# Kernel optimization log

Measured on AMD Instinct MI355X. Metric: run time of the kernel, lower is better.

The kernel has to match this reference:

```python
import jax, jax.numpy as jnp
import numpy as np
from functools import partial

TEMP = 0.07
BN_EPS = 1e-5


def conv1x1(W, x):
    # W: (c_out, c_in), x: (b, c_in, t, h, w) -> (b, c_out, t, h, w)
    return jnp.einsum('oc,bcthw->bothw', W, x)


def dwconv3d(x, W, spatial_dilation):
    # depthwise conv3d, kernel (9,3,3), temporal pad 4, spatial pad = dilation
    rc = x.shape[1]
    d = spatial_dilation
    return jax.lax.conv_general_dilated(
        x, W,
        window_strides=(1, 1, 1),
        padding=[(4, 4), (d, d), (d, d)],
        rhs_dilation=(1, d, d),
        feature_group_count=rc,
        dimension_numbers=('NCDHW', 'OIDHW', 'NCDHW'))


def sk_feat(nx, nseq, seq):
    # nx, nseq, seq: (b, c, t, n). Torch einsum 'bthh,bcth->bcth' takes the
    # DIAGONAL of softmax(aff/T, axis=-1); compute it via logsumexp without
    # materializing the softmax matrix.
    aff = jnp.einsum('bctn,bctm->btnm', nx, nseq) / TEMP          # (b,t,n,n)
    lse = jax.nn.logsumexp(aff, axis=-1)                           # (b,t,n)
    diag = jnp.einsum('bctn,bctn->btn', nx, nseq) / TEMP           # (b,t,n)
    diag_sm = jnp.exp(diag - lse)                                  # (b,t,n)
    return diag_sm[:, None, :, :] * seq                            # (b,c,t,n)


def shift_prev(x):  # seq1: [x[:, :, :1], x[:, :, :-1]]
    return jnp.concatenate([x[:, :, :1], x[:, :, :-1]], axis=2)


def shift_next(x):  # seq2: [x[:, :, 1:], x[:, :, -1:]]
    return jnp.concatenate([x[:, :, 1:], x[:, :, -1:]], axis=2)


def forward(x, W_dc2, W_up2, W_dc, W_sa1, W_sa2, W_sa3, W_back, gamma, beta):
    shortcut = x
    x = conv1x1(W_dc2, x)                                          # (b,c,t,h,w)
    norm = jnp.sqrt(jnp.sum(x * x, axis=1, keepdims=True))
    nx = x / jnp.maximum(norm, 1e-12)                              # F.normalize dim=1
    b, c, t, h, w = x.shape
    n = h * w
    x4 = x.reshape(b, c, t, n)
    nx4 = nx.reshape(b, c, t, n)

    third = jnp.float32(1.0 / 3.0)  # weights2 = ones(3)/3, non-trainable
    feats = (sk_feat(nx4, shift_prev(nx4), shift_prev(x4)) * third
             + sk_feat(nx4, shift_next(nx4), shift_next(x4)) * third
             + sk_feat(nx4, nx4, x4) * third)
    feats = feats.reshape(b, c, t, h, w)

    xx = conv1x1(W_dc, x)                                          # (b, rc, t, h, w)
    agg = (dwconv3d(xx, W_sa1, 1) * third
           + dwconv3d(xx, W_sa2, 2) * third
           + dwconv3d(xx, W_sa3, 3) * third)
    score = jax.nn.relu(conv1x1(W_back, agg))                      # (b,c,t,h,w)

    feats = conv1x1(W_up2, feats * score)
    y = shortcut + feats

    # BatchNorm3d (training-mode batch statistics, biased variance)
    mean = jnp.mean(y, axis=(0, 2, 3, 4), keepdims=True)
    var = jnp.mean((y - mean) ** 2, axis=(0, 2, 3, 4), keepdims=True)
    g = gamma[None, :, None, None, None]
    bta = beta[None, :, None, None, None]
    y = g * (y - mean) / jnp.sqrt(var + BN_EPS) + bta
    return jax.nn.relu(y)


def setup_inputs() -> dict:
    key = jax.random.key(0)
    ks = jax.random.split(key, 10)
    c = 256
    rc = c // 4
    b, t, h, w = 4, 8, 28, 28
    s = 0.05
    return {
        'x': jax.random.normal(ks[0], (b, c, t, h, w), dtype=jnp.float32),
        'W_dc2': jax.random.normal(ks[1], (c, c), dtype=jnp.float32) * s,
        'W_up2': jax.random.normal(ks[2], (c, c), dtype=jnp.float32) * s,
        'W_dc': jax.random.normal(ks[3], (rc, c), dtype=jnp.float32) * s,
        'W_sa1': jax.random.normal(ks[4], (rc, 1, 9, 3, 3), dtype=jnp.float32) * s,
        'W_sa2': jax.random.normal(ks[5], (rc, 1, 9, 3, 3), dtype=jnp.float32) * s,
        'W_sa3': jax.random.normal(ks[6], (rc, 1, 9, 3, 3), dtype=jnp.float32) * s,
        'W_back': jax.random.normal(ks[7], (c, rc), dtype=jnp.float32) * s,
        'gamma': jax.random.uniform(ks[8], (c,), dtype=jnp.float32, minval=0.5, maxval=1.5),
        'beta': jax.random.normal(ks[9], (c,), dtype=jnp.float32) * s,
    }


def reference(x, W_dc2, W_up2, W_dc, W_sa1, W_sa2, W_sa3, W_back, gamma, beta):
    return forward(x, W_dc2, W_up2, W_dc, W_sa1, W_sa2, W_sa3, W_back, gamma, beta)
```

## Files before the change

kernel.cpp:

```cpp
#include <hip/hip_runtime.h>

#define B_ 4
#define C_ 256
#define T_ 8
#define HW_ 784
#define RC_ 64
#define TNH (T_*HW_)
#define BT_ (B_*T_)
#define TEMP_INV 14.28571428571f

typedef __attribute__((ext_vector_type(8))) short bf16x8;
typedef __attribute__((ext_vector_type(4))) float f32x4;

__device__ __forceinline__ ushort f2bf(float f) {
    uint x = __float_as_uint(f);
    uint r = (x + 0x7FFFu + ((x >> 16) & 1u)) >> 16;
    return (ushort)r;
}

#define GL2LDS16(g, l) __builtin_amdgcn_global_load_lds( \
    (const __attribute__((address_space(1))) void*)(g), \
    (__attribute__((address_space(3))) void*)(l), 16, 0, 0)

__global__ __launch_bounds__(256) void k_wcvt(
    const float* __restrict__ w_dc2, const float* __restrict__ w_up2,
    const float* __restrict__ w_dc, const float* __restrict__ w_back,
    ushort* __restrict__ dst)
{
    const int idx = blockIdx.x * 256 + threadIdx.x;
    if (idx >= 163840) return;
    float v;
    if (idx < 65536)       v = w_dc2[idx];
    else if (idx < 131072) v = w_up2[idx - 65536];
    else if (idx < 147456) v = w_dc[idx - 131072];
    else                   v = w_back[idx - 147456];
    dst[idx] = f2bf(v);
}

__global__ __launch_bounds__(256) void k_xpose(
    const float* __restrict__ X, ushort* __restrict__ XT)
{
    __shared__ float xs[256][17];
    const int sl = blockIdx.y, b = sl >> 3, t = sl & 7;
    const int n0 = blockIdx.x * 16;
    const int tid = threadIdx.x;
    {
        const int n_l = tid & 15;
        const int c0 = tid >> 4;
        const float* p = X + (b * C_ * T_ + c0 * T_ + t) * HW_ + n0 + n_l;
        #pragma unroll
        for (int i = 0; i < 16; ++i)
            xs[c0 + 16 * i][n_l] = p[(size_t)16 * i * TNH];
    }
    __syncthreads();
    const int n_l = tid >> 4;
    const int cq = tid & 15;
    union { ushort u[16]; uint4 q[2]; } o;
    #pragma unroll
    for (int i = 0; i < 16; ++i)
        o.u[i] = f2bf(xs[cq * 16 + i][n_l]);
    uint4* dst = (uint4*)(XT + ((size_t)(sl * HW_ + n0 + n_l)) * 256 + cq * 16);
    dst[0] = o.q[0];
    dst[1] = o.q[1];
}

__global__ __launch_bounds__(256) void k_xpose64(
    const float* __restrict__ A, ushort* __restrict__ AT)
{
    __shared__ float xs[64][17];
    const int sl = blockIdx.y, b = sl >> 3, t = sl & 7;
    const int n0 = blockIdx.x * 16;
    const int tid = threadIdx.x;
    {
        const int n_l = tid & 15;
        const int c0 = tid >> 4;
        #pragma unroll
        for (int i = 0; i < 4; ++i)
            xs[c0 + 16 * i][n_l] = A[((size_t)(b * RC_ + c0 + 16 * i) * T_ + t) * HW_ + n0 + n_l];
    }
    __syncthreads();
    const int n_l = tid >> 4;
    const int cq = tid & 15;
    union { ushort u[4]; uint2 q; } o;
    #pragma unroll
    for (int i = 0; i < 4; ++i)
        o.u[i] = f2bf(xs[cq * 4 + i][n_l]);
    *(uint2*)(AT + ((size_t)(sl * HW_ + n0 + n_l)) * 64 + cq * 4) = o.q;
}

template<int MCH, int KK, int MODE>
__global__ __launch_bounds__(256) void k_gemm_cm(
    const ushort* __restrict__ Wsrc, const ushort* __restrict__ XT,
    float* __restrict__ Y, const float* __restrict__ aux)
{
    constexpr int KD = KK * 32;
    constexpr int GPR = KD / 8;
    constexpr int M = MCH * 16;
    __shared__ __align__(16) ushort Bs[2][16 * KD];
    const int sl = blockIdx.y, b = sl >> 3, t = sl & 7;
    const int wid = threadIdx.x >> 6, lane = threadIdx.x & 63;
    const int r = lane & 15, kg = lane >> 4;
    const int tile0_raw = blockIdx.x * 8 + wid * 2;
    const int tile0 = min(tile0_raw, 48), tile1 = min(tile0_raw + 1, 48);

    const short* Ab = (const short*)XT + (size_t)sl * HW_ * KD + kg * 8;
    bf16x8 a0[KK], a1[KK];
    #pragma unroll
    for (int kk = 0; kk < KK; ++kk) {
        a0[kk] = *(const bf16x8*)(Ab + (size_t)(tile0 * 16 + r) * KD + kk * 32);
        a1[kk] = *(const bf16x8*)(Ab + (size_t)(tile1 * 16 + r) * KD + kk * 32);
    }
    #pragma unroll
    for (int kk = 0; kk < KK; ++kk) {
        asm volatile("" : "+v"(a0[kk]));
        asm volatile("" : "+v"(a1[kk]));
    }

    f32x4 nrm0, nrm1;
    if (MODE == 1) {
        nrm0 = *(const f32x4*)&aux[sl * HW_ + tile0 * 16 + kg * 4];
        nrm1 = *(const f32x4*)&aux[sl * HW_ + tile1 * 16 + kg * 4];
    }

    #define STAGE_W(buf, ch) do {                                              \
        if (KK == 8) {                                                         \
            _Pragma("unroll")                                                  \
            for (int e = 0; e < 2; ++e) {                                      \
                const int slot = wid * 128 + e * 64 + lane;                    \
                const int m = slot >> 5;                                       \
                const int j = (slot & 31) ^ (m & 7);                           \
                const ushort* g = Wsrc + (size_t)((ch) * 16 + m) * KD + j * 8; \
                ushort* l = &Bs[buf][(size_t)(wid * 128 + e * 64) * 8];        \
                GL2LDS16(g, l);                                                \
            }                                                                  \
        } else {                                                               \
            if (wid < 2) {                                                     \
                const int slot = wid * 64 + lane;                              \
                const int m = slot >> 3;                                       \
                const int j = (slot & 7) ^ (m & 7);                            \
                const ushort* g = Wsrc + (size_t)((ch) * 16 + m) * KD + j * 8; \
                ushort* l = &Bs[buf][(size_t)(wid * 64) * 8];                  \
                GL2LDS16(g, l);                                                \
            }                                                                  \
        }                                                                      \
    } while (0)

    STAGE_W(0, 0);
    __syncthreads();
    for (int ch = 0; ch < MCH; ++ch) {
        const int cur = ch & 1;
        if (ch + 1 < MCH) STAGE_W(cur ^ 1, ch + 1);
        f32x4 acc0 = {0.f, 0.f, 0.f, 0.f};
        f32x4 acc1 = {0.f, 0.f, 0.f, 0.f};
        #pragma unroll
        for (int kk = 0; kk < KK; ++kk) {
            const int gidx = (kk * 4 + kg) ^ (r & 7);
            bf16x8 bfr = *(const bf16x8*)&Bs[cur][(size_t)(r * GPR + gidx) * 8];
            acc0 = __builtin_amdgcn_mfma_f32_16x16x32_bf16(a0[kk], bfr, acc0, 0, 0, 0);
            acc1 = __builtin_amdgcn_mfma_f32_16x16x32_bf16(a1[kk], bfr, acc1, 0, 0, 0);
        }
        const int o = ch * 16 + r;
        const size_t ybase = ((size_t)(b * M + o) * T_ + t) * HW_;
        if (tile0_raw < 49) {
            const int n0 = tile0_raw * 16 + kg * 4;
            f32x4 v = acc0;
            if (MODE == 1) v *= nrm0;
            if (MODE == 2) v += *(const f32x4*)&aux[((size_t)(b * C_ + o) * T_ + t) * HW_ + n0];
            *(f32x4*)&Y[ybase + n0] = v;
        }
        if (tile0_raw + 1 < 49) {
            const int n0 = (tile0_raw + 1) * 16 + kg * 4;
            f32x4 v = acc1;
            if (MODE == 1) v *= nrm1;
            if (MODE == 2) v += *(const f32x4*)&aux[((size_t)(b * C_ + o) * T_ + t) * HW_ + n0];
            *(f32x4*)&Y[ybase + n0] = v;
        }
        __syncthreads();
    }
    #undef STAGE_W
}

__global__ __launch_bounds__(256) void k_gemm_fs(
    const ushort* __restrict__ Wsrc, const ushort* __restrict__ aggT,
    const float* __restrict__ x1, const float* __restrict__ dsm,
    ushort* __restrict__ fsT)
{
    __shared__ __align__(16) ushort Bs[2][16 * 64];
    const int sl = blockIdx.y, b = sl >> 3, t = sl & 7;
    const int tp = t > 0 ? t - 1 : 0;
    const int tn = t < 7 ? t + 1 : 7;
    const int wid = threadIdx.x >> 6, lane = threadIdx.x & 63;
    const int r = lane & 15, kg = lane >> 4;
    const int tile0_raw = blockIdx.x * 8 + wid * 2;
    const int tile0 = min(tile0_raw, 48), tile1 = min(tile0_raw + 1, 48);

    const short* Ab = (const short*)aggT + (size_t)sl * HW_ * 64 + kg * 8;
    bf16x8 a0[2], a1[2];
    #pragma unroll
    for (int kk = 0; kk < 2; ++kk) {
        a0[kk] = *(const bf16x8*)(Ab + (size_t)(tile0 * 16 + r) * 64 + kk * 32);
        a1[kk] = *(const bf16x8*)(Ab + (size_t)(tile1 * 16 + r) * 64 + kk * 32);
    }
    #pragma unroll
    for (int kk = 0; kk < 2; ++kk) {
        asm volatile("" : "+v"(a0[kk]));
        asm volatile("" : "+v"(a1[kk]));
    }

    #define STAGE_B(buf, ch) do {                                          \
        if (wid < 2) {                                                     \
            const int slot = wid * 64 + lane;                              \
            const int m = slot >> 3;                                       \
            const int j = (slot & 7) ^ (m & 7);                            \
            const ushort* g = Wsrc + (size_t)((ch) * 16 + m) * 64 + j * 8; \
            ushort* l = &Bs[buf][(size_t)(wid * 64) * 8];                  \
            GL2LDS16(g, l);                                                \
        }                                                                  \
    } while (0)

    const float* dp_b = dsm + (0 * BT_ + sl) * HW_;
    const float* dn_b = dsm + (1 * BT_ + sl) * HW_;
    const float* di_b = dsm + (2 * BT_ + sl) * HW_;

    STAGE_B(0, 0);
    __syncthreads();
    for (int ch = 0; ch < 16; ++ch) {
        const int cur = ch & 1;
        if (ch + 1 < 16) STAGE_B(cur ^ 1, ch + 1);
        f32x4 acc0 = {0.f, 0.f, 0.f, 0.f};
        f32x4 acc1 = {0.f, 0.f, 0.f, 0.f};
        #pragma unroll
        for (int kk = 0; kk < 2; ++kk) {
            const int gidx = (kk * 4 + kg) ^ (r & 7);
            bf16x8 bfr = *(const bf16x8*)&Bs[cur][(size_t)(r * 8 + gidx) * 8];
            acc0 = __builtin_amdgcn_mfma_f32_16x16x32_bf16(a0[kk], bfr, acc0, 0, 0, 0);
            acc1 = __builtin_amdgcn_mfma_f32_16x16x32_bf16(a1[kk], bfr, acc1, 0, 0, 0);
        }
        const int o = ch * 16 + r;
        const float* xb = x1 + (size_t)(b * C_ + o) * TNH;
        auto epi = [&](const f32x4& acc, int tileR) {
            const int n0 = tileR * 16 + kg * 4;
            const f32x4 dp = *(const f32x4*)&dp_b[n0];
            const f32x4 dn = *(const f32x4*)&dn_b[n0];
            const f32x4 di = *(const f32x4*)&di_b[n0];
            const f32x4 xp = *(const f32x4*)&xb[tp * HW_ + n0];
            const f32x4 xn = *(const f32x4*)&xb[tn * HW_ + n0];
            const f32x4 xi = *(const f32x4*)&xb[t * HW_ + n0];
            #pragma unroll
            for (int j = 0; j < 4; ++j) {
                const float feats = (dp[j] * xp[j] + dn[j] * xn[j] + di[j] * xi[j]) * (1.f / 3.f);
                const float fs = fmaxf(acc[j], 0.f) * feats;
                fsT[((size_t)sl * HW_ + n0 + j) * 256 + o] = f2bf(fs);
            }
        };
        if (tile0_raw < 49)     epi(acc0, tile0_raw);
        if (tile0_raw + 1 < 49) epi(acc1, tile0_raw + 1);
        __syncthreads();
    }
    #undef STAGE_B
}

__global__ __launch_bounds__(256) void k_invnorm(
    const float* __restrict__ x1, float* __restrict__ invn, float* __restrict__ nrm)
{
    __shared__ float sm[4][64];
    const int sl = blockIdx.y, b = sl >> 3, t = sl & 7;
    const int l = threadIdx.x & 63;
    const int cg = threadIdx.x >> 6;
    const int n = blockIdx.x * 64 + l;
    float s = 0.f;
    if (n < HW_) {
        const float* p = x1 + (b * C_ * T_ + t) * HW_ + n;
        for (int c = cg * 64; c < cg * 64 + 64; ++c) {
            const float v = p[c * TNH];
            s = fmaf(v, v, s);
        }
    }
    sm[cg][l] = s;
    __syncthreads();
    if (threadIdx.x < 64 && n < HW_) {
        const float tot = sm[0][l] + sm[1][l] + sm[2][l] + sm[3][l];
        const float nm = fmaxf(sqrtf(tot), 1e-12f);
        nrm[sl * HW_ + n] = nm;
        invn[sl * HW_ + n] = 1.f / nm;
    }
}

__global__ __launch_bounds__(256) void k_nxT(
    const float* __restrict__ x1, const float* __restrict__ invn,
    ushort* __restrict__ nxT)
{
    __shared__ float xs[256][17];
    __shared__ float inv_s[16];
    const int sl = blockIdx.y, b = sl >> 3, t = sl & 7;
    const int n0 = blockIdx.x * 16;
    const int tid = threadIdx.x;
    {
        const int n_l = tid & 15;
        const int c0 = tid >> 4;
        const float* p = x1 + (b * C_ * T_ + c0 * T_ + t) * HW_ + n0 + n_l;
        #pragma unroll
        for (int i = 0; i < 16; ++i)
            xs[c0 + 16 * i][n_l] = p[(size_t)16 * i * TNH];
        if (tid < 16) inv_s[tid] = invn[sl * HW_ + n0 + tid];
    }
    __syncthreads();
    const int n_l = tid >> 4;
    const int cq = tid & 15;
    const float inv = inv_s[n_l];
    union { ushort u[16]; uint4 q[2]; } o;
    #pragma unroll
    for (int i = 0; i < 16; ++i)
        o.u[i] = f2bf(xs[cq * 16 + i][n_l] * inv);
    uint4* dst = (uint4*)(nxT + ((size_t)(sl * HW_ + n0 + n_l)) * 256 + cq * 16);
    dst[0] = o.q[0];
    dst[1] = o.q[1];
}

__global__ __launch_bounds__(256) void k_affinity_mfma(
    const ushort* __restrict__ nxT, float* __restrict__ sumexp)
{
    __shared__ __align__(16) ushort Bs[2][16 * 256];
    const int sl = blockIdx.y;
    const int s  = blockIdx.z;
    const int b = sl >> 3, t = sl & 7;
    const int t2 = (s == 0) ? (t > 0 ? t - 1 : 0) : (s == 1) ? (t < 7 ? t + 1 : 7) : t;
    const int sl2 = b * 8 + t2;
    const int wid = threadIdx.x >> 6;
    const int lane = threadIdx.x & 63;
    const int r  = lane & 15;
    const int kg = lane >> 4;

    const int tile0_raw = blockIdx.x * 8 + wid * 2;
    const int tile0 = min(tile0_raw, 48);
    const int tile1 = min(tile0_raw + 1, 48);

    const short* Ab = (const short*)nxT + (size_t)sl * HW_ * 256 + kg * 8;
    bf16x8 a0[8], a1[8];
    #pragma unroll
    for (int kk = 0; kk < 8; ++kk) {
        a0[kk] = *(const bf16x8*)(Ab + (size_t)(tile0 * 16 + r) * 256 + kk * 32);
        a1[kk] = *(const bf16x8*)(Ab + (size_t)(tile1 * 16 + r) * 256 + kk * 32);
    }
    #pragma unroll
    for (int kk = 0; kk < 8; ++kk) {
        asm volatile("" : "+v"(a0[kk]));
        asm volatile("" : "+v"(a1[kk]));
    }

    const ushort* Bsrc = nxT + (size_t)sl2 * HW_ * 256;

    #define STAGE_AFF(buf, ch) do {                                           \
        _Pragma("unroll")                                                     \
        for (int e = 0; e < 2; ++e) {                                         \
            const int slot = wid * 128 + e * 64 + lane;                       \
            const int m = slot >> 5;                                          \
            const int j = (slot & 31) ^ (m & 7);                              \
            const ushort* g = Bsrc + (size_t)((ch) * 16 + m) * 256 + j * 8;   \
            ushort* l = &Bs[buf][(size_t)(wid * 128 + e * 64) * 8];           \
            GL2LDS16(g, l);                                                   \
        }                                                                     \
    } while (0)

    float re0[4] = {0.f, 0.f, 0.f, 0.f};
    float re1[4] = {0.f, 0.f, 0.f, 0.f};

    STAGE_AFF(0, 0);
    __syncthreads();
    for (int ch = 0; ch < 49; ++ch) {
        const int cur = ch & 1;
        if (ch + 1 < 49) STAGE_AFF(cur ^ 1, ch + 1);
        f32x4 acc0 = {0.f, 0.f, 0.f, 0.f};
        f32x4 acc1 = {0.f, 0.f, 0.f, 0.f};
        #pragma unroll
        for (int kk = 0; kk < 8; ++kk) {
            const int gidx = (kk * 4 + kg) ^ (r & 7);
            bf16x8 bfr = *(const bf16x8*)&Bs[cur][(size_t)(r * 32 + gidx) * 8];
            acc0 = __builtin_amdgcn_mfma_f32_16x16x32_bf16(a0[kk], bfr, acc0, 0, 0, 0);
            acc1 = __builtin_amdgcn_mfma_f32_16x16x32_bf16(a1[kk], bfr, acc1, 0, 0, 0);
        }
        #pragma unroll
        for (int j = 0; j < 4; ++j) {
            re0[j] += __expf(acc0[j] * TEMP_INV);
            re1[j] += __expf(acc1[j] * TEMP_INV);
        }
        __syncthreads();
    }

    #pragma unroll
    for (int j = 0; j < 4; ++j) {
        float v0 = re0[j], v1 = re1[j];
        v0 += __shfl_xor(v0, 1); v1 += __shfl_xor(v1, 1);
        v0 += __shfl_xor(v0, 2); v1 += __shfl_xor(v1, 2);
        v0 += __shfl_xor(v0, 4); v1 += __shfl_xor(v1, 4);
        v0 += __shfl_xor(v0, 8); v1 += __shfl_xor(v1, 8);
        re0[j] = v0; re1[j] = v1;
    }
    float* dst = sumexp + (s * BT_ + sl) * HW_;
    if ((lane & 15) == 0) {
        if (tile0_raw < 49) {
            #pragma unroll
            for (int j = 0; j < 4; ++j)
                dst[tile0_raw * 16 + kg * 4 + j] = re0[j];
        }
        if (tile0_raw + 1 < 49) {
            #pragma unroll
            for (int j = 0; j < 4; ++j)
                dst[(tile0_raw + 1) * 16 + kg * 4 + j] = re1[j];
        }
    }
    #undef STAGE_AFF
}

__global__ __launch_bounds__(256) void k_diagsm(
    const float* __restrict__ x1, const float* __restrict__ invn,
    const float* __restrict__ sumexp, float* __restrict__ dsm)
{
    __shared__ float sm[3][4][64];
    const int sl = blockIdx.y, b = sl >> 3, t = sl & 7;
    const int l = threadIdx.x & 63;
    const int cg = threadIdx.x >> 6;
    const int n = blockIdx.x * 64 + l;
    const int tp = t > 0 ? t - 1 : 0;
    const int tn = t < 7 ? t + 1 : 7;
    float sp = 0.f, sn2 = 0.f, si = 0.f;
    if (n < HW_) {
        const float* p0 = x1 + (b * C_ * T_ + t) * HW_ + n;
        const float* pp = x1 + (b * C_ * T_ + tp) * HW_ + n;
        const float* pn = x1 + (b * C_ * T_ + tn) * HW_ + n;
        for (int c = cg * 64; c < cg * 64 + 64; ++c) {
            const float v = p0[c * TNH];
            sp  = fmaf(v, pp[c * TNH], sp);
            sn2 = fmaf(v, pn[c * TNH], sn2);
            si  = fmaf(v, v, si);
        }
    }
    sm[0][cg][l] = sp; sm[1][cg][l] = sn2; sm[2][cg][l] = si;
    __syncthreads();
    if (threadIdx.x < 64 && n < HW_) {
        const float d0 = sm[0][0][l] + sm[0][1][l] + sm[0][2][l] + sm[0][3][l];
        const float d1 = sm[1][0][l] + sm[1][1][l] + sm[1][2][l] + sm[1][3][l];
        const float d2 = sm[2][0][l] + sm[2][1][l] + sm[2][2][l] + sm[2][3][l];
        const float it  = invn[sl * HW_ + n];
        const float ip  = invn[(b * T_ + tp) * HW_ + n];
        const float in2 = invn[(b * T_ + tn) * HW_ + n];
        dsm[(0 * BT_ + sl) * HW_ + n] = __expf(d0 * it * ip  * TEMP_INV) / sumexp[(0 * BT_ + sl) * HW_ + n];
        dsm[(1 * BT_ + sl) * HW_ + n] = __expf(d1 * it * in2 * TEMP_INV) / sumexp[(1 * BT_ + sl) * HW_ + n];
        dsm[(2 * BT_ + sl) * HW_ + n] = __expf(d2 * it * it  * TEMP_INV) / sumexp[(2 * BT_ + sl) * HW_ + n];
    }
}

__global__ __launch_bounds__(448) void k_dwconv(
    const float* __restrict__ xx, const float* __restrict__ Wsa1,
    const float* __restrict__ Wsa2, const float* __restrict__ Wsa3,
    float* __restrict__ agg)
{
    __shared__ float xp[8 * 680];
    __shared__ float wl[3][81];
    const int br = blockIdx.x >> 1;
    const int half = blockIdx.x & 1;
    const int h0 = half * 14;
    const int r = br & 63;
    const int tid = threadIdx.x;
    const int base = br * TNH;
    for (int i = tid; i < 8 * 680; i += 448) xp[i] = 0.f;
    if (tid < 243) {
        const int s = tid / 81, k = tid % 81;
        const float* Wp = (s == 0) ? Wsa1 : (s == 1) ? Wsa2 : Wsa3;
        wl[s][k] = Wp[r * 81 + k] * (1.f / 3.f);
    }
    __syncthreads();
    for (int i = tid; i < 8 * 20 * 28; i += 448) {
        const int t = i / 560;
        const int rem = i - t * 560;
        const int row = rem / 28, col = rem - row * 28;
        const int hh = h0 - 3 + row;
        if (hh >= 0 && hh < 28)
            xp[t * 680 + row * 34 + col + 3] = xx[base + t * HW_ + hh * 28 + col];
    }
    __syncthreads();
    if (tid < 392) {
        const int hl = tid / 28, w = tid - hl * 28;
        const float* cen = &xp[(hl + 3) * 34 + (w + 3)];
        float acc[8] = {0.f, 0.f, 0.f, 0.f, 0.f, 0.f, 0.f, 0.f};
        for (int s = 0; s < 3; ++s) {
            const int d = s + 1;
            #pragma unroll
            for (int kh = 0; kh < 3; ++kh) {
                #pragma unroll
                for (int kw = 0; kw < 3; ++kw) {
                    const int off = (kh - 1) * d * 34 + (kw - 1) * d;
                    float wr[9];
                    #pragma unroll
                    for (int kt = 0; kt < 9; ++kt)
                        wr[kt] = wl[s][kt * 9 + kh * 3 + kw];
                    #pragma unroll
                    for (int ts = 0; ts < 8; ++ts) {
                        const float v = cen[ts * 680 + off];
                        #pragma unroll
                        for (int kt = 0; kt < 9; ++kt) {
                            const int t = ts + 4 - kt;
                            if (t >= 0 && t < 8)
                                acc[t] = fmaf(v, wr[kt], acc[t]);
                        }
                    }
                }
            }
        }
        const int p = h0 * 28 + tid;
        #pragma unroll
        for (int t = 0; t < 8; ++t)
            agg[base + t * HW_ + p] = acc[t];
    }
}

__global__ __launch_bounds__(256) void k_bnstats(
    const float* __restrict__ y, const float* __restrict__ gamma,
    const float* __restrict__ beta, float* __restrict__ stats)
{
    __shared__ float sm1[256], sm2[256];
    const int c = blockIdx.x;
    float s1 = 0.f, s2 = 0.f;
    for (int b = 0; b < B_; ++b) {
        const float* p = y + (b * C_ + c) * TNH;
        for (int i = threadIdx.x; i < TNH; i += 256) {
            const float v = p[i];
            s1 += v; s2 = fmaf(v, v, s2);
        }
    }
    sm1[threadIdx.x] = s1; sm2[threadIdx.x] = s2;
    __syncthreads();
    for (int off = 128; off > 0; off >>= 1) {
        if (threadIdx.x < off) {
            sm1[threadIdx.x] += sm1[threadIdx.x + off];
            sm2[threadIdx.x] += sm2[threadIdx.x + off];
        }
        __syncthreads();
    }
    if (threadIdx.x == 0) {
        const float M = (float)(B_ * TNH);
        const float mean = sm1[0] / M;
        const float var = sm2[0] / M - mean * mean;
        const float sc = gamma[c] * rsqrtf(var + 1e-5f);
        stats[c] = sc;
        stats[C_ + c] = beta[c] - mean * sc;
    }
}

__global__ __launch_bounds__(256) void k_bnapply(
    const float* __restrict__ y, const float* __restrict__ stats,
    float* __restrict__ out)
{
    const int total4 = B_ * C_ * TNH / 4;
    for (int i4 = blockIdx.x * 256 + threadIdx.x; i4 < total4; i4 += gridDim.x * 256) {
        float4 v = ((const float4*)y)[i4];
        const int c = (i4 / (TNH / 4)) & 255;
        const float sc = stats[c], bi = stats[C_ + c];
        v.x = fmaxf(fmaf(v.x, sc, bi), 0.f);
        v.y = fmaxf(fmaf(v.y, sc, bi), 0.f);
        v.z = fmaxf(fmaf(v.z, sc, bi), 0.f);
        v.w = fmaxf(fmaf(v.w, sc, bi), 0.f);
        ((float4*)out)[i4] = v;
    }
}

extern "C" void kernel_launch(void* const* d_in, const int* in_sizes, int n_in,
                              void* d_out, int out_size, void* d_ws, size_t ws_size,
                              hipStream_t stream) {
    (void)in_sizes; (void)n_in; (void)out_size; (void)ws_size;
    const float* x      = (const float*)d_in[0];
    const float* W_dc2  = (const float*)d_in[1];
    const float* W_up2  = (const float*)d_in[2];
    const float* W_dc   = (const float*)d_in[3];
    const float* Wsa1   = (const float*)d_in[4];
    const float* Wsa2   = (const float*)d_in[5];
    const float* Wsa3   = (const float*)d_in[6];
    const float* W_back = (const float*)d_in[7];
    const float* gamma  = (const float*)d_in[8];
    const float* beta   = (const float*)d_in[9];
    float* out = (float*)d_out;
    float* ws  = (float*)d_ws;

    const size_t NE = (size_t)B_ * C_ * TNH;
    const size_t NR = (size_t)B_ * RC_ * TNH;
    float* x1     = ws;
    ushort* nxT   = (ushort*)(ws + NE);
    ushort* xT    = (ushort*)(ws + NE + NE / 2);
    float* xx     = ws + 2 * NE;
    float* agg    = xx + NR;
    ushort* aggT  = (ushort*)(agg + NR);
    float* invn   = agg + NR + NR / 2;
    float* nrm    = invn + (size_t)BT_ * HW_;
    float* sumexp = nrm + (size_t)BT_ * HW_;
    float* dsm    = sumexp + 3 * (size_t)BT_ * HW_;
    float* stats  = dsm + 3 * (size_t)BT_ * HW_;
    ushort* Wbf   = (ushort*)(stats + 512);
    ushort* fsT   = xT;

    k_wcvt<<<640, 256, 0, stream>>>(W_dc2, W_up2, W_dc, W_back, Wbf);
    k_xpose<<<dim3(49, 32), 256, 0, stream>>>(x, xT);
    k_gemm_cm<16, 8, 0><<<dim3(7, 32), 256, 0, stream>>>(Wbf, xT, x1, nullptr);
    k_invnorm<<<dim3(13, 32), 256, 0, stream>>>(x1, invn, nrm);
    k_nxT<<<dim3(49, 32), 256, 0, stream>>>(x1, invn, nxT);
    k_affinity_mfma<<<dim3(7, 32, 3), 256, 0, stream>>>(nxT, sumexp);
    k_diagsm<<<dim3(13, 32), 256, 0, stream>>>(x1, invn, sumexp, dsm);
    k_gemm_cm<4, 8, 1><<<dim3(7, 32), 256, 0, stream>>>(Wbf + 131072, nxT, xx, nrm);
    k_dwconv<<<512, 448, 0, stream>>>(xx, Wsa1, Wsa2, Wsa3, agg);
    k_xpose64<<<dim3(49, 32), 256, 0, stream>>>(agg, aggT);
    k_gemm_fs<<<dim3(7, 32), 256, 0, stream>>>(Wbf + 147456, aggT, x1, dsm, fsT);
    k_gemm_cm<16, 8, 2><<<dim3(7, 32), 256, 0, stream>>>(Wbf + 65536, fsT, x1, x);
    k_bnstats<<<256, 256, 0, stream>>>(x1, gamma, beta, stats);
    k_bnapply<<<2048, 256, 0, stream>>>(x1, stats, out);
}
```

Baseline: 259.6 us.

## Share staged key slice across three temporal shifts in affinity kernel

Restructures the affinity kernel so each block stages one key time-slice (t2) into LDS once and multiplies it against the query tiles of the three time slices that use it (t2, t2+1, t2-1). Previously each shift had its own block that restaged the same key data. Each wave now holds one row tile per shift rather than two row tiles for one shift, and the grid drops the shift dimension. This is meant to cut redundant global-to-LDS traffic, at the cost of more A-fragment registers and a different grid shape. At the boundary time steps the same output row is written twice with identical values.

```diff
diff --git a/kernel.cpp b/kernel.cpp
--- a/kernel.cpp
+++ b/kernel.cpp
@@ -321,34 +321,44 @@
     const ushort* __restrict__ nxT, float* __restrict__ sumexp)
 {
     __shared__ __align__(16) ushort Bs[2][16 * 256];
-    const int sl = blockIdx.y;
-    const int s  = blockIdx.z;
-    const int b = sl >> 3, t = sl & 7;
-    const int t2 = (s == 0) ? (t > 0 ? t - 1 : 0) : (s == 1) ? (t < 7 ? t + 1 : 7) : t;
-    const int sl2 = b * 8 + t2;
+    const int bb = blockIdx.y >> 3;
+    const int t2 = blockIdx.y & 7;
+    const int tA0 = t2;
+    const int tA1 = (t2 < 7) ? t2 + 1 : 7;
+    const int tA2 = (t2 > 0) ? t2 - 1 : 0;
+    const int sO0 = 2;
+    const int sO1 = (t2 < 7) ? 0 : 1;
+    const int sO2 = (t2 > 0) ? 1 : 0;
+
     const int wid = threadIdx.x >> 6;
     const int lane = threadIdx.x & 63;
     const int r  = lane & 15;
     const int kg = lane >> 4;
 
-    const int tile0_raw = blockIdx.x * 8 + wid * 2;
-    const int tile0 = min(tile0_raw, 48);
-    const int tile1 = min(tile0_raw + 1, 48);
-
-    const short* Ab = (const short*)nxT + (size_t)sl * HW_ * 256 + kg * 8;
-    bf16x8 a0[8], a1[8];
-    #pragma unroll
-    for (int kk = 0; kk < 8; ++kk) {
-        a0[kk] = *(const bf16x8*)(Ab + (size_t)(tile0 * 16 + r) * 256 + kk * 32);
-        a1[kk] = *(const bf16x8*)(Ab + (size_t)(tile1 * 16 + r) * 256 + kk * 32);
+    const int rt_raw = blockIdx.x * 4 + wid;
+    const int rt = min(rt_raw, 48);
+
+    const short* base16 = (const short*)nxT + ((size_t)(rt * 16 + r)) * 256 + kg * 8;
+    bf16x8 a0[8], a1[8], a2[8];
+    {
+        const short* Ab0 = base16 + (size_t)(bb * 8 + tA0) * HW_ * 256;
+        const short* Ab1 = base16 + (size_t)(bb * 8 + tA1) * HW_ * 256;
+        const short* Ab2 = base16 + (size_t)(bb * 8 + tA2) * HW_ * 256;
+        #pragma unroll
+        for (int kk = 0; kk < 8; ++kk) {
+            a0[kk] = *(const bf16x8*)(Ab0 + kk * 32);
+            a1[kk] = *(const bf16x8*)(Ab1 + kk * 32);
+            a2[kk] = *(const bf16x8*)(Ab2 + kk * 32);
+        }
     }
     #pragma unroll
     for (int kk = 0; kk < 8; ++kk) {
         asm volatile("" : "+v"(a0[kk]));
         asm volatile("" : "+v"(a1[kk]));
-    }
-
-    const ushort* Bsrc = nxT + (size_t)sl2 * HW_ * 256;
+        asm volatile("" : "+v"(a2[kk]));
+    }
+
+    const ushort* Bsrc = nxT + (size_t)(bb * 8 + t2) * HW_ * 256;
 
     #define STAGE_AFF(buf, ch) do {                                           \
         _Pragma("unroll")                                                     \
@@ -364,6 +374,7 @@
 
     float re0[4] = {0.f, 0.f, 0.f, 0.f};
     float re1[4] = {0.f, 0.f, 0.f, 0.f};
+    float re2[4] = {0.f, 0.f, 0.f, 0.f};
 
     STAGE_AFF(0, 0);
     __syncthreads();
@@ -372,41 +383,43 @@
         if (ch + 1 < 49) STAGE_AFF(cur ^ 1, ch + 1);
         f32x4 acc0 = {0.f, 0.f, 0.f, 0.f};
         f32x4 acc1 = {0.f, 0.f, 0.f, 0.f};
+        f32x4 acc2 = {0.f, 0.f, 0.f, 0.f};
         #pragma unroll
         for (int kk = 0; kk < 8; ++kk) {
             const int gidx = (kk * 4 + kg) ^ (r & 7);
             bf16x8 bfr = *(const bf16x8*)&Bs[cur][(size_t)(r * 32 + gidx) * 8];
             acc0 = __builtin_amdgcn_mfma_f32_16x16x32_bf16(a0[kk], bfr, acc0, 0, 0, 0);
             acc1 = __builtin_amdgcn_mfma_f32_16x16x32_bf16(a1[kk], bfr, acc1, 0, 0, 0);
+            acc2 = __builtin_amdgcn_mfma_f32_16x16x32_bf16(a2[kk], bfr, acc2, 0, 0, 0);
         }
         #pragma unroll
         for (int j = 0; j < 4; ++j) {
             re0[j] += __expf(acc0[j] * TEMP_INV);
             re1[j] += __expf(acc1[j] * TEMP_INV);
+            re2[j] += __expf(acc2[j] * TEMP_INV);
         }
         __syncthreads();
     }
 
     #pragma unroll
     for (int j = 0; j < 4; ++j) {
-        float v0 = re0[j], v1 = re1[j];
-        v0 += __shfl_xor(v0, 1); v1 += __shfl_xor(v1, 1);
-        v0 += __shfl_xor(v0, 2); v1 += __shfl_xor(v1, 2);
-        v0 += __shfl_xor(v0, 4); v1 += __shfl_xor(v1, 4);
-        v0 += __shfl_xor(v0, 8); v1 += __shfl_xor(v1, 8);
-        re0[j] = v0; re1[j] = v1;
-    }
-    float* dst = sumexp + (s * BT_ + sl) * HW_;
-    if ((lane & 15) == 0) {
-        if (tile0_raw < 49) {
-            #pragma unroll
-            for (int j = 0; j < 4; ++j)
-                dst[tile0_raw * 16 + kg * 4 + j] = re0[j];
-        }
-        if (tile0_raw + 1 < 49) {
-            #pragma unroll
-            for (int j = 0; j < 4; ++j)
-                dst[(tile0_raw + 1) * 16 + kg * 4 + j] = re1[j];
+        float v0 = re0[j], v1 = re1[j], v2 = re2[j];
+        v0 += __shfl_xor(v0, 1); v1 += __shfl_xor(v1, 1); v2 += __shfl_xor(v2, 1);
+        v0 += __shfl_xor(v0, 2); v1 += __shfl_xor(v1, 2); v2 += __shfl_xor(v2, 2);
+        v0 += __shfl_xor(v0, 4); v1 += __shfl_xor(v1, 4); v2 += __shfl_xor(v2, 4);
+        v0 += __shfl_xor(v0, 8); v1 += __shfl_xor(v1, 8); v2 += __shfl_xor(v2, 8);
+        re0[j] = v0; re1[j] = v1; re2[j] = v2;
+    }
+    if ((lane & 15) == 0 && rt_raw < 49) {
+        const int n0 = rt_raw * 16 + kg * 4;
+        float* d0 = sumexp + (size_t)(sO0 * BT_ + bb * 8 + tA0) * HW_ + n0;
+        float* d1 = sumexp + (size_t)(sO1 * BT_ + bb * 8 + tA1) * HW_ + n0;
+        float* d2 = sumexp + (size_t)(sO2 * BT_ + bb * 8 + tA2) * HW_ + n0;
+        #pragma unroll
+        for (int j = 0; j < 4; ++j) {
+            d0[j] = re0[j];
+            d1[j] = re1[j];
+            d2[j] = re2[j];
         }
     }
     #undef STAGE_AFF
@@ -602,7 +615,7 @@
     k_gemm_cm<16, 8, 0><<<dim3(7, 32), 256, 0, stream>>>(Wbf, xT, x1, nullptr);
     k_invnorm<<<dim3(13, 32), 256, 0, stream>>>(x1, invn, nrm);
     k_nxT<<<dim3(49, 32), 256, 0, stream>>>(x1, invn, nxT);
-    k_affinity_mfma<<<dim3(7, 32, 3), 256, 0, stream>>>(nxT, sumexp);
+    k_affinity_mfma<<<dim3(13, 32), 256, 0, stream>>>(nxT, sumexp);
     k_diagsm<<<dim3(13, 32), 256, 0, stream>>>(x1, invn, sumexp, dsm);
     k_gemm_cm<4, 8, 1><<<dim3(7, 32), 256, 0, stream>>>(Wbf + 131072, nxT, xx, nrm);
     k_dwconv<<<512, 448, 0, stream>>>(xx, Wsa1, Wsa2, Wsa3, agg);
```

Result: no change. 261.1 us (+0.6%).
